# Optimization experiments

Hardware: AMD Instinct MI355X
Metric: run time of the kernel (lower is better)

The kernel has to match this reference:

```python
import jax, jax.numpy as jnp
import numpy as np

EPS = 1e-12  # matches torch F.normalize default eps


def _l2_normalize(x, axis):
    n = jnp.sqrt(jnp.sum(x * x, axis=axis, keepdims=True))
    return x / jnp.maximum(n, EPS)


def _sp_loss(x, r, weight):
    # x, r: [B, C, M, N]; weight: [C]
    B, C, M, N = x.shape
    # trace(matmul(norm_rows(x), norm_rows(r).T)) == sum over rows of cosine sim
    xr = _l2_normalize(x, axis=3)
    rr = _l2_normalize(r, axis=3)
    a_per = jnp.sum(xr * rr, axis=(2, 3)) / M  # [B, C]
    xc = _l2_normalize(x, axis=2)
    rc = _l2_normalize(r, axis=2)
    b_per = jnp.sum(xc * rc, axis=(2, 3)) / N  # [B, C]
    a = jnp.sum(a_per * weight[None, :])
    b = jnp.sum(b_per * weight[None, :])
    return (-a / B) + (-b / B)


def _image_gradients(x):
    # x: [B, C, H, W]
    f_v = x[:, :, :, :-1] - x[:, :, :, 1:]  # [B, C, H, W-1]
    f_h = x[:, :, :-1, :] - x[:, :, 1:, :]  # [B, C, H-1, W]
    return f_v, f_h


def setup_inputs() -> dict:
    key = jax.random.key(0)
    k1, k2 = jax.random.split(key)
    B, C, H, W = 32, 3, 512, 512
    inp = jax.random.normal(k1, (B, C, H, W), dtype=jnp.float32)
    ref = jax.random.normal(k2, (B, C, H, W), dtype=jnp.float32)
    return {"input": inp, "reference": ref}


def reference(input, reference):
    weight = jnp.array([1.0, 1.0, 1.0], dtype=input.dtype)
    iv, ih = _image_gradients(input)
    rv, rh = _image_gradients(reference)
    return _sp_loss(iv, rv, weight) + _sp_loss(ih, rh, weight)
```

## Files before the change

### kernel.cpp

```cpp
#include <hip/hip_runtime.h>


typedef float f32x4 __attribute__((ext_vector_type(4)));
typedef float f32x2 __attribute__((ext_vector_type(2)));

__device__ __forceinline__ f32x2 fma2(f32x2 a, f32x2 b, f32x2 c){
  return __builtin_elementwise_fma(a, b, c);
}

#define DPP_ADD(x, ctrl, rmask) \
  x += __int_as_float(__builtin_amdgcn_update_dpp(0, __float_as_int(x), ctrl, rmask, 0xf, false))

__device__ __forceinline__ float wave_dpp_sum(float x){
  DPP_ADD(x, 0x111, 0xf);
  DPP_ADD(x, 0x112, 0xf);
  DPP_ADD(x, 0x114, 0xf);
  DPP_ADD(x, 0x118, 0xf);
  DPP_ADD(x, 0x142, 0xa);
  DPP_ADD(x, 0x143, 0xc);
  return x;
}

__device__ __forceinline__ float cos_sim(float d, float sx, float sr){
  float nx = fmaxf(sqrtf(sx), 1e-12f);
  float nr = fmaxf(sqrtf(sr), 1e-12f);
  return d / (nx * nr);
}

__global__ __launch_bounds__(512) void gp_uni(
    const float* __restrict__ X, const float* __restrict__ R,
    float* __restrict__ rowPart, float* __restrict__ colPart)
{
  const int bid = blockIdx.x;
  const int p = bid >> 3, q = bid & 7;
  const int tid = threadIdx.x, w = tid >> 6, l = tid & 63;
  const int rg = w >> 1;
  const int wp = w & 1;
  const size_t plane = (size_t)p * (512u * 512u);
  const float* xp = X + plane;
  const float* rp = R + plane;
  const int c  = wp*256 + 4*l;
  const int cn = (c+4 < 512) ? c+4 : 511;
  const bool tlast = (c == 508);
  const int h0 = q*64 + rg*16;

  __shared__ float Abuf[6][512];
  __shared__ float Bbuf[6][512];
  __shared__ float rowbuf[64][2][6];

  f32x2 cv0a={0.f,0.f}, cv0b={0.f,0.f}, cv1a={0.f,0.f}, cv1b={0.f,0.f};
  f32x2 cv2a={0.f,0.f}, cv2b={0.f,0.f}, ch0a={0.f,0.f}, ch0b={0.f,0.f};
  f32x2 ch1a={0.f,0.f}, ch1b={0.f,0.f}, ch2a={0.f,0.f}, ch2b={0.f,0.f};

  const float* xr0 = xp + (size_t)h0*512;
  const float* rr0 = rp + (size_t)h0*512;
  float4 xc4 = *(const float4*)(xr0 + c);
  float4 rc4 = *(const float4*)(rr0 + c);
  float  xhv = xr0[cn], rhv = rr0[cn];

  #pragma unroll 2
  for (int k = 0; k < 16; ++k){
    const int h  = h0 + k;
    const int hn = (h+1 < 512) ? h+1 : 511;
    const float* xr = xp + (size_t)hn*512;
    const float* rr = rp + (size_t)hn*512;
    const float4 nx4 = *(const float4*)(xr + c);
    const float4 nr4 = *(const float4*)(rr + c);
    const float  nxh = xr[cn], nrh = rr[cn];

    const f32x2 ax01 = {xc4.x, xc4.y}, ax23 = {xc4.z, xc4.w};
    const f32x2 ar01 = {rc4.x, rc4.y}, ar23 = {rc4.z, rc4.w};
    const f32x2 bx01 = {nx4.x, nx4.y}, bx23 = {nx4.z, nx4.w};
    const f32x2 br01 = {nr4.x, nr4.y}, br23 = {nr4.z, nr4.w};
    const f32x2 sx01 = {xc4.y, xc4.z}, sx23 = {xc4.w, tlast ? xc4.w : xhv};
    const f32x2 sr01 = {rc4.y, rc4.z}, sr23 = {rc4.w, tlast ? rc4.w : rhv};

    const f32x2 dv01 = ax01 - sx01, dv23 = ax23 - sx23;
    const f32x2 ev01 = ar01 - sr01, ev23 = ar23 - sr23;
    const f32x2 dh01 = ax01 - bx01, dh23 = ax23 - bx23;
    const f32x2 eh01 = ar01 - br01, eh23 = ar23 - br23;

    f32x2 p0v = dv01*ev01; p0v = fma2(dv23, ev23, p0v);
    f32x2 p1v = dv01*dv01; p1v = fma2(dv23, dv23, p1v);
    f32x2 p2v = ev01*ev01; p2v = fma2(ev23, ev23, p2v);
    f32x2 q0v = dh01*eh01; q0v = fma2(dh23, eh23, q0v);
    f32x2 q1v = dh01*dh01; q1v = fma2(dh23, dh23, q1v);
    f32x2 q2v = eh01*eh01; q2v = fma2(eh23, eh23, q2v);

    cv0a = fma2(dv01, ev01, cv0a); cv0b = fma2(dv23, ev23, cv0b);
    cv1a = fma2(dv01, dv01, cv1a); cv1b = fma2(dv23, dv23, cv1b);
    cv2a = fma2(ev01, ev01, cv2a); cv2b = fma2(ev23, ev23, cv2b);
    ch0a = fma2(dh01, eh01, ch0a); ch0b = fma2(dh23, eh23, ch0b);
    ch1a = fma2(dh01, dh01, ch1a); ch1b = fma2(dh23, dh23, ch1b);
    ch2a = fma2(eh01, eh01, ch2a); ch2b = fma2(eh23, eh23, ch2b);

    float p0 = p0v.x + p0v.y, p1 = p1v.x + p1v.y, p2 = p2v.x + p2v.y;
    float q0 = q0v.x + q0v.y, q1 = q1v.x + q1v.y, q2 = q2v.x + q2v.y;

    p0 = wave_dpp_sum(p0); p1 = wave_dpp_sum(p1); p2 = wave_dpp_sum(p2);
    q0 = wave_dpp_sum(q0); q1 = wave_dpp_sum(q1); q2 = wave_dpp_sum(q2);
    if (l == 63){
      const int rr_ = rg*16 + k;
      rowbuf[rr_][wp][0]=p0; rowbuf[rr_][wp][1]=p1; rowbuf[rr_][wp][2]=p2;
      rowbuf[rr_][wp][3]=q0; rowbuf[rr_][wp][4]=q1; rowbuf[rr_][wp][5]=q2;
    }

    xc4 = nx4; rc4 = nr4; xhv = nxh; rhv = nrh;
  }

  if (rg == 0){
    *(float4*)&Abuf[0][c] = make_float4(cv0a.x,cv0a.y,cv0b.x,cv0b.y);
    *(float4*)&Abuf[1][c] = make_float4(cv1a.x,cv1a.y,cv1b.x,cv1b.y);
    *(float4*)&Abuf[2][c] = make_float4(cv2a.x,cv2a.y,cv2b.x,cv2b.y);
    *(float4*)&Abuf[3][c] = make_float4(ch0a.x,ch0a.y,ch0b.x,ch0b.y);
    *(float4*)&Abuf[4][c] = make_float4(ch1a.x,ch1a.y,ch1b.x,ch1b.y);
    *(float4*)&Abuf[5][c] = make_float4(ch2a.x,ch2a.y,ch2b.x,ch2b.y);
  } else if (rg == 1){
    *(float4*)&Bbuf[0][c] = make_float4(cv0a.x,cv0a.y,cv0b.x,cv0b.y);
    *(float4*)&Bbuf[1][c] = make_float4(cv1a.x,cv1a.y,cv1b.x,cv1b.y);
    *(float4*)&Bbuf[2][c] = make_float4(cv2a.x,cv2a.y,cv2b.x,cv2b.y);
    *(float4*)&Bbuf[3][c] = make_float4(ch0a.x,ch0a.y,ch0b.x,ch0b.y);
    *(float4*)&Bbuf[4][c] = make_float4(ch1a.x,ch1a.y,ch1b.x,ch1b.y);
    *(float4*)&Bbuf[5][c] = make_float4(ch2a.x,ch2a.y,ch2b.x,ch2b.y);
  }
  __syncthreads();
  if (rg == 2 || rg == 3){
    float (*buf)[512] = (rg == 2) ? Abuf : Bbuf;
    float4 t;
    t = *(float4*)&buf[0][c]; t.x+=cv0a.x; t.y+=cv0a.y; t.z+=cv0b.x; t.w+=cv0b.y; *(float4*)&buf[0][c]=t;
    t = *(float4*)&buf[1][c]; t.x+=cv1a.x; t.y+=cv1a.y; t.z+=cv1b.x; t.w+=cv1b.y; *(float4*)&buf[1][c]=t;
    t = *(float4*)&buf[2][c]; t.x+=cv2a.x; t.y+=cv2a.y; t.z+=cv2b.x; t.w+=cv2b.y; *(float4*)&buf[2][c]=t;
    t = *(float4*)&buf[3][c]; t.x+=ch0a.x; t.y+=ch0a.y; t.z+=ch0b.x; t.w+=ch0b.y; *(float4*)&buf[3][c]=t;
    t = *(float4*)&buf[4][c]; t.x+=ch1a.x; t.y+=ch1a.y; t.z+=ch1b.x; t.w+=ch1b.y; *(float4*)&buf[4][c]=t;
    t = *(float4*)&buf[5][c]; t.x+=ch2a.x; t.y+=ch2a.y; t.z+=ch2b.x; t.w+=ch2b.y; *(float4*)&buf[5][c]=t;
  }
  __syncthreads();
  {
    const f32x4* A4 = (const f32x4*)Abuf;
    const f32x4* B4 = (const f32x4*)Bbuf;
    f32x4* s4 = (f32x4*)(colPart + (size_t)bid * (6*512));
    for (int idx = tid; idx < 768; idx += 512)
      s4[idx] = A4[idx] + B4[idx];
  }

  if (tid < 64){
    const float a0 = rowbuf[tid][0][0] + rowbuf[tid][1][0];
    const float a1 = rowbuf[tid][0][1] + rowbuf[tid][1][1];
    const float a2 = rowbuf[tid][0][2] + rowbuf[tid][1][2];
    const float b0 = rowbuf[tid][0][3] + rowbuf[tid][1][3];
    const float b1 = rowbuf[tid][0][4] + rowbuf[tid][1][4];
    const float b2 = rowbuf[tid][0][5] + rowbuf[tid][1][5];
    float rv = cos_sim(a0,a1,a2);
    const int h = q*64 + tid;
    float rh = (h < 511) ? cos_sim(b0,b1,b2) : 0.f;
    rv = wave_dpp_sum(rv);
    rh = wave_dpp_sum(rh);
    if (tid == 63){
      rowPart[2*bid+0] = rv;
      rowPart[2*bid+1] = rh;
    }
  }
}

__global__ __launch_bounds__(256) void gp_cols(
    const float* __restrict__ colPart, double* __restrict__ dblk)
{
  const int p = blockIdx.x >> 1;
  const int f = blockIdx.x & 1;
  const int tid = threadIdx.x;
  double acc = 0.0;
  for (int c = tid; c < 512; c += 256){
    float d = 0.f, a = 0.f, b = 0.f;
    #pragma unroll
    for (int s = 0; s < 8; ++s){
      const float* sp = colPart + ((size_t)(p*8 + s) * 6 + f*3) * 512;
      d += sp[c]; a += sp[512 + c]; b += sp[1024 + c];
    }
    acc += (double)cos_sim(d, a, b);
  }
  #pragma unroll
  for (int m = 1; m < 64; m <<= 1) acc += __shfl_xor(acc, m, 64);
  __shared__ double ls[4];
  const int w = tid >> 6, l = tid & 63;
  if (l == 0) ls[w] = acc;
  __syncthreads();
  if (tid == 0) dblk[blockIdx.x] = ls[0] + ls[1] + ls[2] + ls[3];
}

__global__ __launch_bounds__(256) void gp_fin(
    const double* __restrict__ dblk, const float* __restrict__ rowPart,
    int nblk, float* __restrict__ out)
{
  const int tid = threadIdx.x;
  double rv = 0, rh = 0, cv = 0, ch = 0;
  for (int i = tid; i < nblk; i += 256){
    rv += (double)rowPart[2*i];
    rh += (double)rowPart[2*i+1];
  }
  for (int i = tid; i < 192; i += 256){
    if (i & 1) ch += dblk[i]; else cv += dblk[i];
  }
  #pragma unroll
  for (int m = 1; m < 64; m <<= 1){
    rv += __shfl_xor(rv, m, 64); rh += __shfl_xor(rh, m, 64);
    cv += __shfl_xor(cv, m, 64); ch += __shfl_xor(ch, m, 64);
  }
  __shared__ double ls[4][4];
  const int w = tid >> 6, l = tid & 63;
  if (l == 0){ ls[w][0]=rv; ls[w][1]=rh; ls[w][2]=cv; ls[w][3]=ch; }
  __syncthreads();
  if (tid == 0){
    double RV=0, RH=0, CV=0, CH=0;
    #pragma unroll
    for (int i = 0; i < 4; ++i){ RV+=ls[i][0]; RH+=ls[i][1]; CV+=ls[i][2]; CH+=ls[i][3]; }
    const double t = RV/512.0 + RH/511.0 + CV/511.0 + CH/512.0;
    out[0] = (float)(-t / 32.0);
  }
}

extern "C" void kernel_launch(void* const* d_in, const int* in_sizes, int n_in,
                              void* d_out, int out_size, void* d_ws, size_t ws_size,
                              hipStream_t stream) {
  const float* X = (const float*)d_in[0];
  const float* R = (const float*)d_in[1];
  float* out = (float*)d_out;

  float*  colPart = (float*)d_ws;
  float*  rowPart = colPart + (size_t)768*6*512;
  double* dblk    = (double*)(rowPart + (size_t)768*2);

  gp_uni <<<dim3(768), dim3(512), 0, stream>>>(X, R, rowPart, colPart);
  gp_cols<<<dim3(192), dim3(256), 0, stream>>>(colPart, dblk);
  gp_fin <<<dim3(1),   dim3(256), 0, stream>>>(dblk, rowPart, 768, out);
}
```

Measured before the change: 47.37 us.

## Merge column and final reductions via atomic ticket; shorten per-row DPP reduction

Fuses the column-reduce and final-reduce kernels into one launch. The last block to take an atomic ticket performs the final sum, which removes a kernel launch but adds a memset before the main kernel. Separately, the per-row wave reduction now stops at 16-lane row sums and writes four partials per wave to shared memory, dropping the cross-row DPP steps at the cost of more LDS stores and reads in the epilogue.

```diff
diff --git a/kernel.cpp b/kernel.cpp
--- a/kernel.cpp
+++ b/kernel.cpp
@@ -10,6 +10,14 @@
 
 #define DPP_ADD(x, ctrl, rmask) \
   x += __int_as_float(__builtin_amdgcn_update_dpp(0, __float_as_int(x), ctrl, rmask, 0xf, false))
+
+__device__ __forceinline__ float dpp_psum16(float x){
+  DPP_ADD(x, 0x111, 0xf);
+  DPP_ADD(x, 0x112, 0xf);
+  DPP_ADD(x, 0x114, 0xf);
+  DPP_ADD(x, 0x118, 0xf);
+  return x;
+}
 
 __device__ __forceinline__ float wave_dpp_sum(float x){
   DPP_ADD(x, 0x111, 0xf);
@@ -46,7 +54,7 @@
 
   __shared__ float Abuf[6][512];
   __shared__ float Bbuf[6][512];
-  __shared__ float rowbuf[64][2][6];
+  __shared__ float rowbuf[64][2][4][8];
 
   f32x2 cv0a={0.f,0.f}, cv0b={0.f,0.f}, cv1a={0.f,0.f}, cv1b={0.f,0.f};
   f32x2 cv2a={0.f,0.f}, cv2b={0.f,0.f}, ch0a={0.f,0.f}, ch0b={0.f,0.f};
@@ -97,12 +105,12 @@
     float p0 = p0v.x + p0v.y, p1 = p1v.x + p1v.y, p2 = p2v.x + p2v.y;
     float q0 = q0v.x + q0v.y, q1 = q1v.x + q1v.y, q2 = q2v.x + q2v.y;
 
-    p0 = wave_dpp_sum(p0); p1 = wave_dpp_sum(p1); p2 = wave_dpp_sum(p2);
-    q0 = wave_dpp_sum(q0); q1 = wave_dpp_sum(q1); q2 = wave_dpp_sum(q2);
-    if (l == 63){
-      const int rr_ = rg*16 + k;
-      rowbuf[rr_][wp][0]=p0; rowbuf[rr_][wp][1]=p1; rowbuf[rr_][wp][2]=p2;
-      rowbuf[rr_][wp][3]=q0; rowbuf[rr_][wp][4]=q1; rowbuf[rr_][wp][5]=q2;
+    p0 = dpp_psum16(p0); p1 = dpp_psum16(p1); p2 = dpp_psum16(p2);
+    q0 = dpp_psum16(q0); q1 = dpp_psum16(q1); q2 = dpp_psum16(q2);
+    if ((l & 15) == 15){
+      float* dst = &rowbuf[rg*16 + k][wp][l >> 4][0];
+      *(float4*)dst       = make_float4(p0, p1, p2, q0);
+      *(float2*)(dst + 4) = make_float2(q1, q2);
     }
 
     xc4 = nx4; rc4 = nr4; xhv = nxh; rhv = nrh;
@@ -144,12 +152,18 @@
   }
 
   if (tid < 64){
-    const float a0 = rowbuf[tid][0][0] + rowbuf[tid][1][0];
-    const float a1 = rowbuf[tid][0][1] + rowbuf[tid][1][1];
-    const float a2 = rowbuf[tid][0][2] + rowbuf[tid][1][2];
-    const float b0 = rowbuf[tid][0][3] + rowbuf[tid][1][3];
-    const float b1 = rowbuf[tid][0][4] + rowbuf[tid][1][4];
-    const float b2 = rowbuf[tid][0][5] + rowbuf[tid][1][5];
+    float a0=0.f,a1=0.f,a2=0.f,b0=0.f,b1=0.f,b2=0.f;
+    #pragma unroll
+    for (int wp_ = 0; wp_ < 2; ++wp_){
+      #pragma unroll
+      for (int g = 0; g < 4; ++g){
+        const float* src = &rowbuf[tid][wp_][g][0];
+        const float4 sA = *(const float4*)src;
+        const float2 sB = *(const float2*)(src + 4);
+        a0 += sA.x; a1 += sA.y; a2 += sA.z;
+        b0 += sA.w; b1 += sB.x; b2 += sB.y;
+      }
+    }
     float rv = cos_sim(a0,a1,a2);
     const int h = q*64 + tid;
     float rh = (h < 511) ? cos_sim(b0,b1,b2) : 0.f;
@@ -162,12 +176,17 @@
   }
 }
 
-__global__ __launch_bounds__(256) void gp_cols(
-    const float* __restrict__ colPart, double* __restrict__ dblk)
+__global__ __launch_bounds__(256) void gp_fin2(
+    const float* __restrict__ colPart, const float* __restrict__ rowPart,
+    double* __restrict__ dblk, unsigned int* __restrict__ ticket,
+    float* __restrict__ out)
 {
-  const int p = blockIdx.x >> 1;
-  const int f = blockIdx.x & 1;
+  const int bid = blockIdx.x;
+  const int p = bid >> 1;
+  const int f = bid & 1;
   const int tid = threadIdx.x;
+  const int w = tid >> 6, l = tid & 63;
+
   double acc = 0.0;
   for (int c = tid; c < 512; c += 256){
     float d = 0.f, a = 0.f, b = 0.f;
@@ -181,40 +200,46 @@
   #pragma unroll
   for (int m = 1; m < 64; m <<= 1) acc += __shfl_xor(acc, m, 64);
   __shared__ double ls[4];
-  const int w = tid >> 6, l = tid & 63;
   if (l == 0) ls[w] = acc;
   __syncthreads();
-  if (tid == 0) dblk[blockIdx.x] = ls[0] + ls[1] + ls[2] + ls[3];
-}
-
-__global__ __launch_bounds__(256) void gp_fin(
-    const double* __restrict__ dblk, const float* __restrict__ rowPart,
-    int nblk, float* __restrict__ out)
-{
-  const int tid = threadIdx.x;
-  double rv = 0, rh = 0, cv = 0, ch = 0;
-  for (int i = tid; i < nblk; i += 256){
-    rv += (double)rowPart[2*i];
-    rh += (double)rowPart[2*i+1];
-  }
-  for (int i = tid; i < 192; i += 256){
-    if (i & 1) ch += dblk[i]; else cv += dblk[i];
-  }
-  #pragma unroll
-  for (int m = 1; m < 64; m <<= 1){
-    rv += __shfl_xor(rv, m, 64); rh += __shfl_xor(rh, m, 64);
-    cv += __shfl_xor(cv, m, 64); ch += __shfl_xor(ch, m, 64);
-  }
-  __shared__ double ls[4][4];
-  const int w = tid >> 6, l = tid & 63;
-  if (l == 0){ ls[w][0]=rv; ls[w][1]=rh; ls[w][2]=cv; ls[w][3]=ch; }
-  __syncthreads();
+
+  __shared__ unsigned int my;
   if (tid == 0){
-    double RV=0, RH=0, CV=0, CH=0;
+    const double total = ls[0] + ls[1] + ls[2] + ls[3];
+    atomicExch((unsigned long long*)&dblk[bid],
+               (unsigned long long)__double_as_longlong(total));
+    __threadfence();
+    my = atomicAdd(ticket, 1u);
+  }
+  __syncthreads();
+
+  if (my == 191){
+    double rv = 0, rh = 0, cv = 0, ch = 0;
+    for (int i = tid; i < 768; i += 256){
+      rv += (double)rowPart[2*i];
+      rh += (double)rowPart[2*i+1];
+    }
+    for (int i = tid; i < 192; i += 256){
+      const unsigned long long u =
+        atomicAdd((unsigned long long*)&dblk[i], 0ull);
+      const double v = __longlong_as_double((long long)u);
+      if (i & 1) ch += v; else cv += v;
+    }
     #pragma unroll
-    for (int i = 0; i < 4; ++i){ RV+=ls[i][0]; RH+=ls[i][1]; CV+=ls[i][2]; CH+=ls[i][3]; }
-    const double t = RV/512.0 + RH/511.0 + CV/511.0 + CH/512.0;
-    out[0] = (float)(-t / 32.0);
+    for (int m = 1; m < 64; m <<= 1){
+      rv += __shfl_xor(rv, m, 64); rh += __shfl_xor(rh, m, 64);
+      cv += __shfl_xor(cv, m, 64); ch += __shfl_xor(ch, m, 64);
+    }
+    __shared__ double fs[4][4];
+    if (l == 0){ fs[w][0]=rv; fs[w][1]=rh; fs[w][2]=cv; fs[w][3]=ch; }
+    __syncthreads();
+    if (tid == 0){
+      double RV=0, RH=0, CV=0, CH=0;
+      #pragma unroll
+      for (int i = 0; i < 4; ++i){ RV+=fs[i][0]; RH+=fs[i][1]; CV+=fs[i][2]; CH+=fs[i][3]; }
+      const double t = RV/512.0 + RH/511.0 + CV/511.0 + CH/512.0;
+      out[0] = (float)(-t / 32.0);
+    }
   }
 }
 
@@ -228,8 +253,9 @@
   float*  colPart = (float*)d_ws;
   float*  rowPart = colPart + (size_t)768*6*512;
   double* dblk    = (double*)(rowPart + (size_t)768*2);
-
+  unsigned int* ticket = (unsigned int*)(dblk + 192);
+
+  hipMemsetAsync(ticket, 0, 4, stream);
   gp_uni <<<dim3(768), dim3(512), 0, stream>>>(X, R, rowPart, colPart);
-  gp_cols<<<dim3(192), dim3(256), 0, stream>>>(colPart, dblk);
-  gp_fin <<<dim3(1),   dim3(256), 0, stream>>>(dblk, rowPart, 768, out);
-}
+  gp_fin2<<<dim3(192), dim3(256), 0, stream>>>(colPart, rowPart, dblk, ticket, out);
+}
```

After: 54.04 us. 1.14x slower.
